# Kernel optimization log

Hardware: AMD Instinct MI355X
Metric: run time of the kernel (lower is better)

The kernel has to match this reference:

```python
import jax, jax.numpy as jnp
import numpy as np
from jax import lax

GROUPS = 8            # _resolve_groups(256, 8) == 8
EPS = 1e-5            # GroupNorm default eps
TOPK_RATIO = 0.2
MEAN_W, TOPK_W = 0.7, 0.3
DMG_THRESH = 0.5
DN = ('NCHW', 'OIHW', 'NCHW')


def _normalize(p, axis=1):
    # clamp_min(1e-8) / clamp_min(1e-8).sum().clamp_min(1e-8)
    p = jnp.maximum(p, 1e-8)
    return p / jnp.maximum(p.sum(axis=axis, keepdims=True), 1e-8)


def _conv_head(x, w1, gn_s, gn_b, w2, b2):
    # Conv3x3(no bias) -> GroupNorm(8) -> GELU(exact) -> Dropout(eval: identity) -> Conv1x1
    h = lax.conv_general_dilated(x, w1, (1, 1), 'SAME', dimension_numbers=DN)
    B, C, H, W = h.shape
    hg = h.reshape(B, GROUPS, C // GROUPS, H, W)
    mu = jnp.mean(hg, axis=(2, 3, 4), keepdims=True)
    var = jnp.var(hg, axis=(2, 3, 4), keepdims=True)
    h = ((hg - mu) * lax.rsqrt(var + EPS)).reshape(B, C, H, W)
    h = h * gn_s[None, :, None, None] + gn_b[None, :, None, None]
    h = jax.nn.gelu(h, approximate=False)
    return lax.conv_general_dilated(h, w2, (1, 1), 'SAME', dimension_numbers=DN) + b2[None, :, None, None]


def _forward(feature_map, target_mask, dw1, dgs, dgb, dw2, db2, sw1, sgs, sgb, sw2, sb2):
    dmg_logit = _conv_head(feature_map, dw1, dgs, dgb, dw2, db2)      # [B,1,H,W]
    corn_logits = _conv_head(feature_map, sw1, sgs, sgb, sw2, sb2)    # [B,2,H,W]

    # CORN dense decode: threshold probs = cumprod(sigmoid), classes = K+1
    t = jnp.cumprod(jax.nn.sigmoid(corn_logits), axis=1)              # [B,2,H,W]
    sev = jnp.concatenate([1.0 - t[:, :1], t[:, :-1] - t[:, 1:], t[:, -1:]], axis=1)  # [B,3,H,W]
    sev = _normalize(sev, axis=1)

    p_dmg = jax.nn.sigmoid(dmg_logit)                                 # [B,1,H,W]
    pix = jnp.concatenate([1.0 - p_dmg, p_dmg * sev], axis=1)         # [B,4,H,W]
    pix = _normalize(pix, axis=1)

    sev_pred = jnp.argmax(sev, axis=1) + 1                            # [B,H,W]
    pred_labels = jnp.where(p_dmg[:, 0] >= DMG_THRESH, sev_pred, 0)

    # target_mask already at feature resolution -> nearest resize is identity
    valid = target_mask > 0.5                                         # [B,1,H,W] bool
    B, C, H, W = pix.shape
    N = H * W
    flat = pix.transpose(0, 2, 3, 1).reshape(B, N, C)                 # [B,N,C]
    mf = valid.reshape(B, N)                                          # [B,N]
    cnt = mf.sum(axis=1)                                              # [B] int
    uniform = jnp.full((B, C), 1.0 / C, dtype=flat.dtype)

    # masked mean
    denom = jnp.maximum(cnt, 1).astype(flat.dtype)[:, None]
    mean_p = (flat * mf[..., None]).sum(axis=1) / denom
    mean_p = jnp.where((cnt == 0)[:, None], uniform, mean_p)
    mean_p = _normalize(mean_p, axis=1)

    # masked top-k mean via descending sort + cumsum gather (probs >= 0, invalid -> -1)
    masked = jnp.where(mf[..., None], flat, jnp.asarray(-1.0, flat.dtype))
    srt = -jnp.sort(-masked, axis=1)                                  # descending [B,N,C]
    csum = jnp.cumsum(srt, axis=1)
    k = jnp.clip(jnp.round(cnt.astype(jnp.float32) * TOPK_RATIO).astype(jnp.int32), 1, jnp.maximum(cnt, 1))
    idx = jnp.broadcast_to((k - 1)[:, None, None], (B, 1, C))
    topk_p = jnp.take_along_axis(csum, idx, axis=1)[:, 0] / k.astype(flat.dtype)[:, None]
    topk_p = jnp.where((cnt == 0)[:, None], uniform, topk_p)
    topk_p = _normalize(topk_p, axis=1)

    agg = _normalize(MEAN_W * mean_p + TOPK_W * topk_p, axis=1)
    agg_labels = jnp.argmax(agg, axis=1)

    return (dmg_logit, corn_logits, pix, pred_labels, mean_p, topk_p, agg, agg_labels)


def setup_inputs() -> dict:
    key = jax.random.key(0)
    ks = jax.random.split(key, 8)
    B, Cin, Ch, H, W = 8, 256, 256, 128, 128
    inp = {
        'feature_map': jax.random.normal(ks[0], (B, Cin, H, W), jnp.float32),
        'target_mask': jax.random.uniform(ks[1], (B, 1, H, W), jnp.float32),
        # damage head: Conv3x3 -> GN -> Conv1x1 (1 out)
        'dw1': jax.random.normal(ks[2], (Ch, Cin, 3, 3), jnp.float32) * 0.05,
        'dgs': jnp.ones((Ch,), jnp.float32),
        'dgb': jnp.zeros((Ch,), jnp.float32),
        'dw2': jax.random.normal(ks[3], (1, Ch, 1, 1), jnp.float32) * 0.05,
        'db2': jnp.zeros((1,), jnp.float32),
        # severity head: Conv3x3 -> GN -> Conv1x1 (2 thresholds)
        'sw1': jax.random.normal(ks[4], (Ch, Cin, 3, 3), jnp.float32) * 0.05,
        'sgs': jnp.ones((Ch,), jnp.float32),
        'sgb': jnp.zeros((Ch,), jnp.float32),
        'sw2': jax.random.normal(ks[5], (2, Ch, 1, 1), jnp.float32) * 0.05,
        'sb2': jnp.zeros((2,), jnp.float32),
    }
    return inp


def reference(feature_map, target_mask, dw1, dgs, dgb, dw2, db2, sw1, sgs, sgb, sw2, sb2):
    return _forward(feature_map, target_mask, dw1, dgs, dgb, dw2, db2, sw1, sgs, sgb, sw2, sb2)
```

## Files before the change

### kernel.cpp

```cpp
#include <hip/hip_runtime.h>
#include <hip/hip_bf16.h>

#define BB   8
#define CIN  256
#define CHN  256
#define HH   128
#define WWD  128
#define HW   (HH * WWD)
#define GRP_ELEMS ((size_t)32 * HW)

#define FLAG_DL   4e-3f
#define FLAG_GAP  1.5e-3f

#define BO_DSUM1   0
#define BO_DSUM2   1024
#define BO_FSTAT1  2048
#define BO_FSTAT2  2560
#define BO_DSTAT1  3072
#define BO_DSTAT2  4096
#define BO_MEAN    5120
#define BO_CNT     5248
#define BO_TOPK    5280
#define BO_FLAGC   5408
#define MEMSET_BYTES 8192
#define BO_WL      8192
#define WLCAP      32768

#define XP_OFF    139264ull
#define XP_BYTES  67108864ull
#define HB_OFF    (XP_OFF + XP_BYTES)
#define HB_BYTES  134217728ull
#define WH_OFF    (HB_OFF + HB_BYTES)
#define WT_BYTES  1179648ull
#define WL_OFF    (WH_OFF + WT_BYTES)
#define WT32_OFF  (WL_OFF + WT_BYTES)
#define WT32_BYTES 4718592ull
#define MFMA_NEED (WT32_OFF + WT32_BYTES)

#define O_DMG   0
#define O_CORN  131072
#define O_PIX   393216
#define O_LAB   917504
#define O_MEAN  1048576
#define O_TOPK  1048608
#define O_AGG   1048640
#define O_ALAB  1048672

typedef __attribute__((ext_vector_type(8))) _Float16 f16x8;
typedef __attribute__((ext_vector_type(4))) float f32x4;

__device__ inline ushort f2h(float f) {
    _Float16 h = (_Float16)f;
    union { _Float16 h; ushort u; } c; c.h = h; return c.u;
}
__device__ inline float h2f(ushort u) {
    union { ushort u; _Float16 h; } c; c.u = u; return (float)c.h;
}

__device__ inline void store4v(float* p, float a, float b, float c, float d) {
    *(float4*)p = make_float4(a, b, c, d);
}
__device__ inline void store4v(__hip_bfloat16* p, float a, float b, float c, float d) {
    p[0] = __float2bfloat16(a); p[1] = __float2bfloat16(b);
    p[2] = __float2bfloat16(c); p[3] = __float2bfloat16(d);
}
__device__ inline float ldv(const float* p) { return *p; }
__device__ inline float ldv(const __hip_bfloat16* p) { return __bfloat162float(*p); }


__global__ __launch_bounds__(256) void pack_x_f16(
    const float* __restrict__ x, ushort* __restrict__ Xh)
{
    int bid = blockIdx.x;
    int cc = bid & 7;
    int y  = (bid >> 3) & 127;
    int b  = bid >> 10;
    __shared__ ushort tile[32][137];
    const int tid = threadIdx.x;
    for (int i = tid; i < 1024; i += 256) {
        int ci = i >> 5;
        int x4 = (i & 31) << 2;
        float4 v = *(const float4*)&x[(((size_t)b * 256 + cc * 32 + ci) * 128 + y) * 128 + x4];
        tile[ci][x4 + 0] = f2h(v.x);
        tile[ci][x4 + 1] = f2h(v.y);
        tile[ci][x4 + 2] = f2h(v.z);
        tile[ci][x4 + 3] = f2h(v.w);
    }
    __syncthreads();
    ushort* dst = Xh + ((((size_t)b * 128 + y) * 8 + cc) << 12);
    for (int i = tid; i < 512; i += 256) {
        int xx  = i >> 2;
        int ci0 = (i & 3) << 3;
        ushort tmp[8];
#pragma unroll
        for (int j = 0; j < 8; j++) tmp[j] = tile[ci0 + j][xx];
        *(uint4*)&dst[i << 3] = *(uint4*)tmp;
    }
}

__global__ __launch_bounds__(256) void transpose_w(
    const float* __restrict__ w, ushort* __restrict__ Whh,
    ushort* __restrict__ Whl, float* __restrict__ Wt32)
{
    __shared__ float lt[8][33];
    int idx = blockIdx.x * 256 + threadIdx.x;
    int tap = idx >> 16;
    int rem = idx & 65535;
    int cc  = rem >> 13;
    int co  = (rem >> 5) & 255;
    int ci5 = rem & 31;
    int ci  = cc * 32 + ci5;
    float v = w[((size_t)co * 256 + ci) * 9 + tap];
    ushort h = f2h(v);
    int sidx = (((tap * 8 + cc) * 16 + (co >> 4)) << 9)
             + (((co & 15) + ((ci5 >> 3) << 4)) << 3) + (ci5 & 7);
    Whh[sidx] = h;
    Whl[sidx] = f2h(v - h2f(h));
    lt[threadIdx.x >> 5][ci5] = v;
    __syncthreads();
    int co_base = (blockIdx.x * 8) & 255;
    int ci5w = threadIdx.x >> 3;
    int j    = threadIdx.x & 7;
    Wt32[((size_t)tap * 256 + cc * 32 + ci5w) * 256 + co_base + j] = lt[j][ci5w];
}

__device__ __forceinline__ void gld16(const void* g, void* l)
{
    __builtin_amdgcn_global_load_lds(
        (const __attribute__((address_space(1))) void*)g,
        (__attribute__((address_space(3))) void*)l, 16, 0, 0);
}

__device__ __forceinline__ void issue_b_slice(
    const ushort* __restrict__ Whh, const ushort* __restrict__ Whl,
    ushort* dst, int u, int co0, int tid, int wb)
{
    const int su  = u / 3;
    const int kxu = u - su * 3;
    const int tap = ((su >> 3) * 3) + kxu;
    const int cc  = su & 7;
    const size_t sbase = ((size_t)((tap * 8 + cc) * 16 + (co0 >> 4)) << 9);
    const ushort* s0 = Whh + sbase;
    const ushort* s1 = Whl + sbase;
#pragma unroll
    for (int k = 0; k < 2; k++)
        gld16(s0 + (k * 256 + tid) * 8, dst + (size_t)(k * 256 + wb) * 8);
#pragma unroll
    for (int k = 0; k < 2; k++)
        gld16(s1 + (k * 256 + tid) * 8, dst + 4096 + (size_t)(k * 256 + wb) * 8);
}

__device__ __forceinline__ void issue_a_slice(
    const ushort* __restrict__ Xh, const ushort* __restrict__ zb,
    ushort* dst, int b, int y, int sn, int tid, int wb)
{
    const int kyn = sn >> 3, ccn = sn & 7;
    const int rown = y + kyn - 1;
    const bool rv = (unsigned)rown < 128u;
    const ushort* base = rv ? (Xh + ((((size_t)b * 128 + rown) * 8 + ccn) << 12)) : zb;
#pragma unroll
    for (int k = 0; k < 2; k++) {
        int idx = k * 256 + tid;
        int xi  = (idx + 4) >> 2;
        int q   = (idx & 3) ^ ((xi >> 1) & 3);
        int off = rv ? ((xi - 1) * 32 + q * 8) : (idx * 8);
        gld16(base + off, dst + 32 + (size_t)(k * 256 + wb) * 8);
    }
}

__global__ __launch_bounds__(256, 3) void conv3x3_mfma(
    const ushort* __restrict__ Xh, const ushort* __restrict__ Whh,
    const ushort* __restrict__ Whl, const ushort* __restrict__ zb,
    float* __restrict__ hout, double* __restrict__ sums)
{
    __shared__ ushort a_lds[2][4160];
    __shared__ ushort b_lds[2][8192];
    __shared__ float sred[8];

    const int bxr = blockIdx.x;
    const int y   = bxr >> 3;
    const int b   = bxr & 7;
    const int co0 = blockIdx.y << 7;
    const int tid  = threadIdx.x;
    const int lane = tid & 63;
    const int wb   = tid & 192;
    const int wv   = tid >> 6;
    const int m = lane & 15;
    const int q = lane >> 4;
    const int wpx = (wv & 1) << 6;
    const int wco = (wv >> 1) << 6;
    const int g0  = wco >> 4;

    if (tid < 8) sred[tid] = 0.f;
    if (tid < 16) {
        int tg = tid >> 2, p4 = tid & 3;
        ushort* r = &a_lds[tg >> 1][(tg & 1) ? (129 * 32) : 0];
        *(uint4*)(r + p4 * 8) = make_uint4(0u, 0u, 0u, 0u);
    }

    f32x4 acc[4][4];
#pragma unroll
    for (int f = 0; f < 4; f++)
#pragma unroll
        for (int g = 0; g < 4; g++) acc[f][g] = (f32x4){0.f, 0.f, 0.f, 0.f};

    issue_a_slice(Xh, zb, a_lds[0], b, y, 0, tid, wb);
    issue_b_slice(Whh, Whl, b_lds[0], 0, co0, tid, wb);
    asm volatile("s_waitcnt lgkmcnt(0)" ::: "memory");

    for (int s = 0; s < 24; s++) {
        const ushort* acur = a_lds[s & 1];
#pragma unroll
        for (int kx = 0; kx < 3; kx++) {
            const int t = 3 * s + kx;
            asm volatile("" ::: "memory");
            __builtin_amdgcn_s_barrier();
            {
                int u = t + 1;
                int ub = u & 1;
                if (u > 71) u = 71;
                issue_b_slice(Whh, Whl, b_lds[ub], u, co0, tid, wb);
            }
            if (kx == 0) {
                int sn = s + 1;
                int ab = sn & 1;
                if (sn > 23) sn = 23;
                issue_a_slice(Xh, zb, a_lds[ab], b, y, sn, tid, wb);
            }
            if (kx == 2) asm volatile("s_waitcnt vmcnt(4)" ::: "memory");
            else         asm volatile("s_waitcnt vmcnt(6)" ::: "memory");
            __builtin_amdgcn_s_barrier();
            asm volatile("" ::: "memory");

            const ushort* bb = b_lds[t & 1];
            f16x8 ah[4], bh[4], bl[4];
#pragma unroll
            for (int f = 0; f < 4; f++) {
                int row = wpx + f * 16 + kx + m;
                ah[f] = *(const f16x8*)(acur + row * 32
                        + ((q ^ ((row >> 1) & 3)) << 3));
            }
#pragma unroll
            for (int g = 0; g < 4; g++) {
                int off = ((g0 + g) << 9) + (lane << 3);
                bh[g] = *(const f16x8*)&bb[off];
                bl[g] = *(const f16x8*)&bb[4096 + off];
            }
            __builtin_amdgcn_s_setprio(1);
#pragma unroll
            for (int f = 0; f < 4; f++)
#pragma unroll
                for (int g = 0; g < 4; g++)
                    acc[f][g] = __builtin_amdgcn_mfma_f32_16x16x32_f16(ah[f], bh[g], acc[f][g], 0, 0, 0);
#pragma unroll
            for (int f = 0; f < 4; f++)
#pragma unroll
                for (int g = 0; g < 4; g++)
                    acc[f][g] = __builtin_amdgcn_mfma_f32_16x16x32_f16(ah[f], bl[g], acc[f][g], 0, 0, 0);
            __builtin_amdgcn_s_setprio(0);
        }
    }

    float s0 = 0.f, q0 = 0.f, s1 = 0.f, q1 = 0.f;
#pragma unroll
    for (int f = 0; f < 4; f++) {
#pragma unroll
        for (int g = 0; g < 4; g++) {
            f32x4 v = acc[f][g];
            float a = v.x + v.y + v.z + v.w;
            float qq = v.x * v.x + v.y * v.y + v.z * v.z + v.w * v.w;
            if (g < 2) { s0 += a; q0 += qq; } else { s1 += a; q1 += qq; }
            int px = wpx + f * 16 + q * 4;
            int co = co0 + wco + g * 16 + m;
            *(f32x4*)&hout[((size_t)(b * 256 + co) * 128 + y) * 128 + px] = v;
        }
    }
    int gl = wco >> 5;
    atomicAdd(&sred[gl],     s0);
    atomicAdd(&sred[gl + 1], s1);
    atomicAdd(&sred[4 + gl],     q0);
    atomicAdd(&sred[4 + gl + 1], q1);
    __syncthreads();
    if (tid < 4) atomicAdd(&sums[b * 8 + (co0 >> 5) + tid], (double)sred[tid]);
    else if (tid < 8) atomicAdd(&sums[64 + b * 8 + (co0 >> 5) + tid - 4], (double)sred[tid]);
}

template <typename HT>
__global__ __launch_bounds__(256) void conv3x3_gn_stats(
    const float* __restrict__ x, const float* __restrict__ w,
    HT* __restrict__ hout, double* __restrict__ sums)
{
    __shared__ float in_lds[8][3][132];
    __shared__ float w_lds[8][9][68];
    __shared__ float sred[2], qred[2];

    const int bx  = blockIdx.x;
    const int y   = bx & (HH - 1);
    const int b   = bx >> 7;
    const int co0 = blockIdx.y << 6;
    const int tid = threadIdx.x;
    if (tid < 2) { sred[tid] = 0.f; qred[tid] = 0.f; }
    const int tco = (tid & 15) << 2;
    const int tox = (tid >> 4) << 3;

    float acc[4][8];
#pragma unroll
    for (int i = 0; i < 4; i++)
#pragma unroll
        for (int j = 0; j < 8; j++) acc[i][j] = 0.f;

    const float* xb = x + (size_t)b * CIN * HW;
    for (int c0 = 0; c0 < CIN; c0 += 8) {
        __syncthreads();
        for (int i = tid; i < 8 * 3 * 130; i += 256) {
            int ci  = i / 390;
            int rem = i - ci * 390;
            int r   = rem / 130;
            int cx  = rem - r * 130;
            int gy  = y + r - 1;
            int gx  = cx - 1;
            float v = 0.f;
            if ((unsigned)gy < HH && (unsigned)gx < WWD)
                v = xb[(size_t)(c0 + ci) * HW + gy * WWD + gx];
            in_lds[ci][r][cx] = v;
        }
        for (int i = tid; i < 64 * 72; i += 256) {
            int co = i / 72;
            int kk = i - co * 72;
            int ci = kk / 9;
            int k9 = kk - ci * 9;
            w_lds[ci][k9][co] = w[((size_t)(co0 + co) * CIN + (c0 + ci)) * 9 + k9];
        }
        __syncthreads();
#pragma unroll
        for (int ci = 0; ci < 8; ci++) {
#pragma unroll
            for (int ky = 0; ky < 3; ky++) {
                const float* rowp = &in_lds[ci][ky][tox];
                float4 a0 = *(const float4*)rowp;
                float4 a1 = *(const float4*)(rowp + 4);
                float2 a2 = *(const float2*)(rowp + 8);
                float in10[10] = {a0.x, a0.y, a0.z, a0.w,
                                  a1.x, a1.y, a1.z, a1.w, a2.x, a2.y};
#pragma unroll
                for (int kx = 0; kx < 3; kx++) {
                    float4 wv = *(const float4*)&w_lds[ci][ky * 3 + kx][tco];
#pragma unroll
                    for (int ox = 0; ox < 8; ox++) {
                        float iv = in10[ox + kx];
                        acc[0][ox] = fmaf(iv, wv.x, acc[0][ox]);
                        acc[1][ox] = fmaf(iv, wv.y, acc[1][ox]);
                        acc[2][ox] = fmaf(iv, wv.z, acc[2][ox]);
                        acc[3][ox] = fmaf(iv, wv.w, acc[3][ox]);
                    }
                }
            }
        }
    }

    float s = 0.f, qv = 0.f;
#pragma unroll
    for (int oc = 0; oc < 4; oc++)
#pragma unroll
        for (int ox = 0; ox < 8; ox++) { float v = acc[oc][ox]; s += v; qv = fmaf(v, v, qv); }
#pragma unroll
    for (int oc = 0; oc < 4; oc++) {
        size_t base = ((size_t)(b * CHN + co0 + tco + oc)) * HW + y * WWD + tox;
        store4v(hout + base,     acc[oc][0], acc[oc][1], acc[oc][2], acc[oc][3]);
        store4v(hout + base + 4, acc[oc][4], acc[oc][5], acc[oc][6], acc[oc][7]);
    }
    const int gsel = tco >> 5;
    atomicAdd(&sred[gsel], s);
    atomicAdd(&qred[gsel], qv);
    __syncthreads();
    if (tid < 2) {
        int grp = (co0 >> 5) + tid;
        atomicAdd(&sums[b * 8 + grp],      (double)sred[tid]);
        atomicAdd(&sums[64 + b * 8 + grp], (double)qred[tid]);
    }
}

__global__ void gn_finalize(const double* __restrict__ dsums,
                            float* __restrict__ fstats, double* __restrict__ dstats)
{
    int i = threadIdx.x;
    if (i < 64) {
        double inv = 1.0 / (double)GRP_ELEMS;
        double mu  = dsums[i] * inv;
        double ex2 = dsums[64 + i] * inv;
        double var = ex2 - mu * mu;
        double rs  = 1.0 / sqrt(var + 1e-5);
        fstats[i]      = (float)mu;
        fstats[64 + i] = (float)rs;
        dstats[i]      = mu;
        dstats[64 + i] = rs;
    }
}

template <typename HT>
__global__ __launch_bounds__(256) void gn_head(
    const HT* __restrict__ hbuf,
    const float* __restrict__ gs, const float* __restrict__ gb,
    const float* __restrict__ w2, const float* __restrict__ b2,
    const float* __restrict__ stats,
    float* __restrict__ out, int nout)
{
    __shared__ float sc[256], sh[256], w2s[2][256];
    const int b = blockIdx.y;
    const int p = blockIdx.x * 256 + threadIdx.x;
    {
        int c = threadIdx.x;
        float mu = stats[b * 8 + (c >> 5)];
        float rs = stats[64 + b * 8 + (c >> 5)];
        float s  = gs[c] * rs;
        sc[c] = s;
        sh[c] = gb[c] - mu * s;
        w2s[0][c] = w2[c];
        w2s[1][c] = (nout > 1) ? w2[256 + c] : 0.f;
    }
    __syncthreads();
    const HT* hp = hbuf + (size_t)b * CHN * HW + p;
    float a0 = 0.f, a1 = 0.f;
#pragma unroll 4
    for (int c = 0; c < 256; c++) {
        float v = ldv(hp + (size_t)c * HW);
        v = fmaf(v, sc[c], sh[c]);
        float g = 0.5f * v * (1.f + erff(v * 0.70710678118654752440f));
        a0 = fmaf(g, w2s[0][c], a0);
        a1 = fmaf(g, w2s[1][c], a1);
    }
    out[(size_t)b * nout * HW + p] = a0 + b2[0];
    if (nout > 1) out[(size_t)b * nout * HW + HW + p] = a1 + b2[1];
}

__global__ __launch_bounds__(256) void decode_kernel(
    float* __restrict__ outw, const float* __restrict__ mask,
    float* __restrict__ meanacc, float* __restrict__ cntacc,
    int* __restrict__ flagcnt, int* __restrict__ wl)
{
    const int b = blockIdx.y;
    const int p = blockIdx.x * 256 + threadIdx.x;

    float dl = outw[O_DMG + b * HW + p];
    float c0 = outw[O_CORN + (b * 2 + 0) * HW + p];
    float c1 = outw[O_CORN + (b * 2 + 1) * HW + p];

    float s0 = 1.f / (1.f + expf(-c0));
    float s1 = 1.f / (1.f + expf(-c1));
    float t0 = s0, t1 = s0 * s1;
    float e0 = fmaxf(1.f - t0, 1e-8f);
    float e1 = fmaxf(t0 - t1, 1e-8f);
    float e2 = fmaxf(t1, 1e-8f);
    float es = fmaxf(e0 + e1 + e2, 1e-8f);
    e0 /= es; e1 /= es; e2 /= es;

    float pd = 1.f / (1.f + expf(-dl));
    float q0 = fmaxf(1.f - pd, 1e-8f);
    float q1 = fmaxf(pd * e0, 1e-8f);
    float q2 = fmaxf(pd * e1, 1e-8f);
    float q3 = fmaxf(pd * e2, 1e-8f);
    float qs = fmaxf(q0 + q1 + q2 + q3, 1e-8f);
    q0 /= qs; q1 /= qs; q2 /= qs; q3 /= qs;

    outw[O_PIX + ((size_t)b * 4 + 0) * HW + p] = q0;
    outw[O_PIX + ((size_t)b * 4 + 1) * HW + p] = q1;
    outw[O_PIX + ((size_t)b * 4 + 2) * HW + p] = q2;
    outw[O_PIX + ((size_t)b * 4 + 3) * HW + p] = q3;

    int am = 0; float bv = e0;
    if (e1 > bv) { bv = e1; am = 1; }
    if (e2 > bv) { bv = e2; am = 2; }
    outw[O_LAB + b * HW + p] = (pd >= 0.5f) ? (float)(am + 1) : 0.f;

    bool flag = (fabsf(dl) < FLAG_DL);
    {
        float top1 = e0, top2 = fmaxf(e1, e2);
        if (e1 > top1) { top1 = e1; top2 = fmaxf(e0, e2); }
        if (e2 > top1) { top1 = e2; top2 = fmaxf(e0, e1); }
        if ((top1 - top2 < FLAG_GAP) && (dl > -FLAG_DL)) flag = true;
    }
    if (flag) {
        int idx = atomicAdd(flagcnt, 1);
        if (idx < WLCAP) wl[idx] = b * HW + p;
    }

    bool valid = mask[b * HW + p] > 0.5f;
    float vm = valid ? 1.f : 0.f;
    float v0 = valid ? q0 : 0.f, v1 = valid ? q1 : 0.f;
    float v2 = valid ? q2 : 0.f, v3 = valid ? q3 : 0.f;

#pragma unroll
    for (int o = 32; o; o >>= 1) {
        v0 += __shfl_down(v0, o); v1 += __shfl_down(v1, o);
        v2 += __shfl_down(v2, o); v3 += __shfl_down(v3, o);
        vm += __shfl_down(vm, o);
    }
    __shared__ float racc[5];
    if (threadIdx.x < 5) racc[threadIdx.x] = 0.f;
    __syncthreads();
    if ((threadIdx.x & 63) == 0) {
        atomicAdd(&racc[0], v0); atomicAdd(&racc[1], v1);
        atomicAdd(&racc[2], v2); atomicAdd(&racc[3], v3);
        atomicAdd(&racc[4], vm);
    }
    __syncthreads();
    if (threadIdx.x < 4) atomicAdd(&meanacc[b * 4 + threadIdx.x], racc[threadIdx.x]);
    if (threadIdx.x == 4) atomicAdd(&cntacc[b], racc[4]);
}

__global__ __launch_bounds__(256) void fixup_labels(
    const float* __restrict__ x, const float* __restrict__ Wt32,
    const float* __restrict__ dgs, const float* __restrict__ dgb,
    const float* __restrict__ dw2, const float* __restrict__ db2,
    const float* __restrict__ sgs, const float* __restrict__ sgb,
    const float* __restrict__ sw2, const float* __restrict__ sb2,
    const double* __restrict__ dstat1, const double* __restrict__ dstat2,
    const int* __restrict__ wl, const int* __restrict__ wcnt,
    float* __restrict__ out)
{
    __shared__ float xp[2304];
    __shared__ double dpart[4][256];
    __shared__ double wred[3][4];

    int count = *wcnt;
    if (count > WLCAP) count = WLCAP;
    const int tid  = threadIdx.x;
    const int lane = tid & 63;
    const int wv   = tid >> 6;
    const int c4   = lane << 2;
    const int j0   = wv * 576;

    for (int pix = blockIdx.x; pix < count; pix += gridDim.x) {
        __syncthreads();
        const int pid = wl[pix];
        const int b = pid >> 14, yy = (pid >> 7) & 127, xx = pid & 127;
        for (int i = tid; i < 2304; i += 256) {
            int t = i >> 8, ci = i & 255;
            int ky = t / 3, kx = t - ky * 3;
            int gy = yy + ky - 1, gx = xx + kx - 1;
            float v = 0.f;
            if ((unsigned)gy < 128u && (unsigned)gx < 128u)
                v = x[(((size_t)b * 256 + ci) * 128 + gy) * 128 + gx];
            xp[i] = v;
        }
        __syncthreads();

        for (int head = 0; head < 2; head++) {
            const float* gs  = head ? sgs : dgs;
            const float* gb  = head ? sgb : dgb;
            const float* w2  = head ? sw2 : dw2;
            const double* st = head ? dstat2 : dstat1;
            const float* wt  = Wt32 + (size_t)head * 589824;

            double a0 = 0.0, a1 = 0.0, a2 = 0.0, a3 = 0.0;
            for (int jc = 0; jc < 576; jc += 8) {
                float4 wv4[8];
#pragma unroll
                for (int u = 0; u < 8; u++)
                    wv4[u] = *(const float4*)&wt[(size_t)(j0 + jc + u) * 256 + c4];
#pragma unroll
                for (int u = 0; u < 8; u++) {
                    double xv = (double)xp[j0 + jc + u];
                    a0 += xv * (double)wv4[u].x;
                    a1 += xv * (double)wv4[u].y;
                    a2 += xv * (double)wv4[u].z;
                    a3 += xv * (double)wv4[u].w;
                }
            }
            dpart[wv][c4]     = a0;
            dpart[wv][c4 + 1] = a1;
            dpart[wv][c4 + 2] = a2;
            dpart[wv][c4 + 3] = a3;
            __syncthreads();

            {
                const int c = tid;
                double h = dpart[0][c] + dpart[1][c] + dpart[2][c] + dpart[3][c];
                double mu = st[b * 8 + (c >> 5)];
                double rs = st[64 + b * 8 + (c >> 5)];
                double v = (h - mu) * rs * (double)gs[c] + (double)gb[c];
                double g = 0.5 * v * (1.0 + erf(v * 0.70710678118654752440));
                double r0 = g * (double)w2[c];
#pragma unroll
                for (int o = 32; o; o >>= 1) r0 += __shfl_down(r0, o);
                if (lane == 0) wred[head][wv] = r0;
                if (head == 1) {
                    double r1 = g * (double)w2[256 + c];
#pragma unroll
                    for (int o = 32; o; o >>= 1) r1 += __shfl_down(r1, o);
                    if (lane == 0) wred[2][wv] = r1;
                }
            }
            __syncthreads();
        }

        if (tid == 0) {
            double dlv = wred[0][0] + wred[0][1] + wred[0][2] + wred[0][3] + (double)db2[0];
            double c0v = wred[1][0] + wred[1][1] + wred[1][2] + wred[1][3] + (double)sb2[0];
            double c1v = wred[2][0] + wred[2][1] + wred[2][2] + wred[2][3] + (double)sb2[1];
            double s0 = 1.0 / (1.0 + exp(-c0v));
            double s1 = 1.0 / (1.0 + exp(-c1v));
            double t0 = s0, t1 = s0 * s1;
            double e0 = fmax(1.0 - t0, 1e-8);
            double e1 = fmax(t0 - t1, 1e-8);
            double e2 = fmax(t1, 1e-8);
            int am = 0; double bv = e0;
            if (e1 > bv) { bv = e1; am = 1; }
            if (e2 > bv) { bv = e2; am = 2; }
            out[O_LAB + pid] = (dlv >= 0.0) ? (float)(am + 1) : 0.f;
        }
    }
}

__global__ __launch_bounds__(256) void topk_kernel(
    const float* __restrict__ outw, const float* __restrict__ mask,
    const float* __restrict__ cntacc, float* __restrict__ topkout)
{
    const int b = blockIdx.x >> 2;
    const int c = blockIdx.x & 3;
    const int tid = threadIdx.x;

    __shared__ int hist[256];
    __shared__ unsigned s_prefix;
    __shared__ int s_want;
    __shared__ float s_red[4];
    __shared__ int s_redi[4];

    float cntf = cntacc[b];
    int cnt = (int)cntf;
    int k = (int)rintf(cntf * 0.2f);
    if (k < 1) k = 1;
    int kmax = cnt > 1 ? cnt : 1;
    if (k > kmax) k = kmax;

    if (tid == 0) { s_prefix = 0u; s_want = k; }

    const float* pv = outw + O_PIX + ((size_t)b * 4 + c) * HW;
    const float* pm = mask + (size_t)b * HW;

    unsigned uv[64];
#pragma unroll
    for (int j = 0; j < 64; j++) {
        int p = tid + (j << 8);
        float v = (pm[p] > 0.5f) ? pv[p] : -1.0f;
        unsigned bits = __float_as_uint(v);
        uv[j] = (bits & 0x80000000u) ? ~bits : (bits | 0x80000000u);
    }

    for (int pass = 0; pass < 4; pass++) {
        hist[tid] = 0;
        __syncthreads();
        const int shift = 24 - 8 * pass;
        const unsigned pmask = pass ? (0xFFFFFFFFu << (shift + 8)) : 0u;
        const unsigned prefix = s_prefix;
#pragma unroll
        for (int j = 0; j < 64; j++) {
            unsigned u = uv[j];
            if ((u & pmask) == prefix) atomicAdd(&hist[(u >> shift) & 255], 1);
        }
        __syncthreads();
        if (tid == 0) {
            int want = s_want;
            int bin = 255;
            while (bin > 0) {
                int h = hist[bin];
                if (want <= h) break;
                want -= h;
                bin--;
            }
            s_want = want;
            s_prefix = prefix | ((unsigned)bin << shift);
        }
        __syncthreads();
    }
    const unsigned tau = s_prefix;

    float sgt = 0.f; int cgt = 0;
#pragma unroll
    for (int j = 0; j < 64; j++) {
        unsigned u = uv[j];
        if (u > tau) {
            unsigned bits = (u & 0x80000000u) ? (u & 0x7FFFFFFFu) : ~u;
            sgt += __uint_as_float(bits);
            cgt++;
        }
    }
#pragma unroll
    for (int o = 32; o; o >>= 1) { sgt += __shfl_down(sgt, o); cgt += __shfl_down(cgt, o); }
    if ((tid & 63) == 0) { s_red[tid >> 6] = sgt; s_redi[tid >> 6] = cgt; }
    __syncthreads();
    if (tid == 0) {
        float S = s_red[0] + s_red[1] + s_red[2] + s_red[3];
        int   C = s_redi[0] + s_redi[1] + s_redi[2] + s_redi[3];
        unsigned tb = (tau & 0x80000000u) ? (tau & 0x7FFFFFFFu) : ~tau;
        float tf = __uint_as_float(tb);
        float total = S + (float)(k - C) * tf;
        topkout[b * 4 + c] = total / (float)k;
    }
}

__device__ inline void norm4(float* p)
{
    float a = fmaxf(p[0], 1e-8f), b = fmaxf(p[1], 1e-8f);
    float c = fmaxf(p[2], 1e-8f), d = fmaxf(p[3], 1e-8f);
    float s = fmaxf(a + b + c + d, 1e-8f);
    p[0] = a / s; p[1] = b / s; p[2] = c / s; p[3] = d / s;
}

__global__ void final_kernel(const float* __restrict__ meanacc,
                             const float* __restrict__ cntacc,
                             const float* __restrict__ topkv,
                             float* __restrict__ outw)
{
    int b = threadIdx.x;
    if (b >= 8) return;
    float cnt = cntacc[b];
    bool zero = (cnt == 0.f);
    float denom = fmaxf(cnt, 1.f);
    float m[4], t[4], a[4];
#pragma unroll
    for (int c = 0; c < 4; c++) {
        m[c] = zero ? 0.25f : meanacc[b * 4 + c] / denom;
        t[c] = zero ? 0.25f : topkv[b * 4 + c];
    }
    norm4(m); norm4(t);
#pragma unroll
    for (int c = 0; c < 4; c++) a[c] = 0.7f * m[c] + 0.3f * t[c];
    norm4(a);
    int am = 0; float bv = a[0];
#pragma unroll
    for (int c = 1; c < 4; c++) if (a[c] > bv) { bv = a[c]; am = c; }
#pragma unroll
    for (int c = 0; c < 4; c++) {
        outw[O_MEAN + b * 4 + c] = m[c];
        outw[O_TOPK + b * 4 + c] = t[c];
        outw[O_AGG  + b * 4 + c] = a[c];
    }
    outw[O_ALAB + b] = (float)am;
}

extern "C" void kernel_launch(void* const* d_in, const int* in_sizes, int n_in,
                              void* d_out, int out_size, void* d_ws, size_t ws_size,
                              hipStream_t stream)
{
    (void)in_sizes; (void)n_in; (void)out_size;
    const float* x    = (const float*)d_in[0];
    const float* mask = (const float*)d_in[1];
    const float* dw1  = (const float*)d_in[2];
    const float* dgs  = (const float*)d_in[3];
    const float* dgb  = (const float*)d_in[4];
    const float* dw2  = (const float*)d_in[5];
    const float* db2  = (const float*)d_in[6];
    const float* sw1  = (const float*)d_in[7];
    const float* sgs  = (const float*)d_in[8];
    const float* sgb  = (const float*)d_in[9];
    const float* sw2  = (const float*)d_in[10];
    const float* sb2  = (const float*)d_in[11];
    float* out = (float*)d_out;

    char* wsb = (char*)d_ws;
    double* dsum1  = (double*)(wsb + BO_DSUM1);
    double* dsum2  = (double*)(wsb + BO_DSUM2);
    float*  fstat1 = (float*)(wsb + BO_FSTAT1);
    float*  fstat2 = (float*)(wsb + BO_FSTAT2);
    double* dstat1 = (double*)(wsb + BO_DSTAT1);
    double* dstat2 = (double*)(wsb + BO_DSTAT2);
    float*  meanacc = (float*)(wsb + BO_MEAN);
    float*  cntacc  = (float*)(wsb + BO_CNT);
    float*  topkv   = (float*)(wsb + BO_TOPK);
    int*    flagc   = (int*)(wsb + BO_FLAGC);
    int*    wl      = (int*)(wsb + BO_WL);

    hipMemsetAsync(d_ws, 0, MEMSET_BYTES + 8192, stream);

    dim3 pgrid(64, BB);

    if (ws_size >= MFMA_NEED) {
        ushort* Xh   = (ushort*)(wsb + XP_OFF);
        float*  hb   = (float*)(wsb + HB_OFF);
        ushort* Whh  = (ushort*)(wsb + WH_OFF);
        ushort* Whl  = (ushort*)(wsb + WL_OFF);
        float*  Wt32 = (float*)(wsb + WT32_OFF);
        const ushort* zb = (const ushort*)(wsb + BO_WL);

        pack_x_f16<<<8192, 256, 0, stream>>>(x, Xh);

        dim3 cgrid(1024, 2);
        transpose_w<<<2304, 256, 0, stream>>>(dw1, Whh, Whl, Wt32);
        conv3x3_mfma<<<cgrid, 256, 0, stream>>>(Xh, Whh, Whl, zb, hb, dsum1);
        gn_finalize<<<1, 64, 0, stream>>>(dsum1, fstat1, dstat1);
        gn_head<float><<<pgrid, 256, 0, stream>>>(hb, dgs, dgb, dw2, db2,
                                                  fstat1, out + O_DMG, 1);
        transpose_w<<<2304, 256, 0, stream>>>(sw1, Whh, Whl, Wt32 + 589824);
        conv3x3_mfma<<<cgrid, 256, 0, stream>>>(Xh, Whh, Whl, zb, hb, dsum2);
        gn_finalize<<<1, 64, 0, stream>>>(dsum2, fstat2, dstat2);
        gn_head<float><<<pgrid, 256, 0, stream>>>(hb, sgs, sgb, sw2, sb2,
                                                  fstat2, out + O_CORN, 2);

        decode_kernel<<<pgrid, 256, 0, stream>>>(out, mask, meanacc, cntacc, flagc, wl);
        fixup_labels<<<512, 256, 0, stream>>>(x, Wt32, dgs, dgb, dw2, db2,
                                              sgs, sgb, sw2, sb2,
                                              dstat1, dstat2, wl, flagc, out);
        topk_kernel<<<32, 256, 0, stream>>>(out, mask, cntacc, topkv);
        final_kernel<<<1, 64, 0, stream>>>(meanacc, cntacc, topkv, out);
    } else {
        void* hbuf = wsb + XP_OFF;
        dim3 cgrid(HH * BB, CHN / 64);
        const size_t needF32 = XP_OFF + (size_t)BB * CHN * HW * sizeof(float);
        if (ws_size >= needF32) {
            conv3x3_gn_stats<float><<<cgrid, 256, 0, stream>>>(x, dw1, (float*)hbuf, dsum1);
            gn_finalize<<<1, 64, 0, stream>>>(dsum1, fstat1, dstat1);
            gn_head<float><<<pgrid, 256, 0, stream>>>((float*)hbuf, dgs, dgb, dw2, db2,
                                                      fstat1, out + O_DMG, 1);
            conv3x3_gn_stats<float><<<cgrid, 256, 0, stream>>>(x, sw1, (float*)hbuf, dsum2);
            gn_finalize<<<1, 64, 0, stream>>>(dsum2, fstat2, dstat2);
            gn_head<float><<<pgrid, 256, 0, stream>>>((float*)hbuf, sgs, sgb, sw2, sb2,
                                                      fstat2, out + O_CORN, 2);
        } else {
            conv3x3_gn_stats<__hip_bfloat16><<<cgrid, 256, 0, stream>>>(x, dw1, (__hip_bfloat16*)hbuf, dsum1);
            gn_finalize<<<1, 64, 0, stream>>>(dsum1, fstat1, dstat1);
            gn_head<__hip_bfloat16><<<pgrid, 256, 0, stream>>>((__hip_bfloat16*)hbuf, dgs, dgb, dw2, db2,
                                                               fstat1, out + O_DMG, 1);
            conv3x3_gn_stats<__hip_bfloat16><<<cgrid, 256, 0, stream>>>(x, sw1, (__hip_bfloat16*)hbuf, dsum2);
            gn_finalize<<<1, 64, 0, stream>>>(dsum2, fstat2, dstat2);
            gn_head<__hip_bfloat16><<<pgrid, 256, 0, stream>>>((__hip_bfloat16*)hbuf, sgs, sgb, sw2, sb2,
                                                               fstat2, out + O_CORN, 2);
        }
        decode_kernel<<<pgrid, 256, 0, stream>>>(out, mask, meanacc, cntacc, flagc, wl);
        topk_kernel<<<32, 256, 0, stream>>>(out, mask, cntacc, topkv);
        final_kernel<<<1, 64, 0, stream>>>(meanacc, cntacc, topkv, out);
    }
}
```

Before: 1.260 ms.

## Merge both conv heads into one MFMA launch with separate hidden buffers

Both 3x3 conv heads now run in a single MFMA kernel launch with four column tiles: two per head, each with its own weights and hidden buffer. GroupNorm finalize and the GN/GELU/1x1 head also each run once for both heads. This removes serialized launches and the tail idle time between the two convs, and it doubles the grid so the GPU is kept busier. The cost is a second 128 MB hidden buffer, which raises workspace demand and memory traffic. The per-channel loop unroll also goes from 4 to 16.

```diff
diff --git a/kernel.cpp b/kernel.cpp
--- a/kernel.cpp
+++ b/kernel.cpp
@@ -31,11 +31,14 @@
 #define HB_OFF    (XP_OFF + XP_BYTES)
 #define HB_BYTES  134217728ull
 #define WH_OFF    (HB_OFF + HB_BYTES)
-#define WT_BYTES  1179648ull
-#define WL_OFF    (WH_OFF + WT_BYTES)
-#define WT32_OFF  (WL_OFF + WT_BYTES)
+#define WT1_ELEMS 589824
+#define WH2_BYTES 2359296ull
+#define WL2_OFF   (WH_OFF + WH2_BYTES)
+#define WT32_OFF  (WL2_OFF + WH2_BYTES)
 #define WT32_BYTES 4718592ull
-#define MFMA_NEED (WT32_OFF + WT32_BYTES)
+#define HB2_OFF   (WT32_OFF + WT32_BYTES)
+#define NEED_B    (WT32_OFF + WT32_BYTES)
+#define NEED_A    (HB2_OFF + HB_BYTES)
 
 #define O_DMG   0
 #define O_CORN  131072
@@ -168,10 +171,12 @@
     }
 }
 
+template <int MERGED>
 __global__ __launch_bounds__(256, 3) void conv3x3_mfma(
     const ushort* __restrict__ Xh, const ushort* __restrict__ Whh,
     const ushort* __restrict__ Whl, const ushort* __restrict__ zb,
-    float* __restrict__ hout, double* __restrict__ sums)
+    float* __restrict__ hb1, float* __restrict__ hb2,
+    double* __restrict__ sums, int headfix)
 {
     __shared__ ushort a_lds[2][4160];
     __shared__ ushort b_lds[2][8192];
@@ -180,7 +185,14 @@
     const int bxr = blockIdx.x;
     const int y   = bxr >> 3;
     const int b   = bxr & 7;
-    const int co0 = blockIdx.y << 7;
+    const int by  = blockIdx.y;
+    const int head = MERGED ? (by >> 1) : headfix;
+    const int co0  = MERGED ? ((by & 1) << 7) : (by << 7);
+    const ushort* WhhH = Whh + head * WT1_ELEMS;
+    const ushort* WhlH = Whl + head * WT1_ELEMS;
+    float* hout = head ? hb2 : hb1;
+    double* sumsH = sums + head * 128;
+
     const int tid  = threadIdx.x;
     const int lane = tid & 63;
     const int wb   = tid & 192;
@@ -205,7 +217,7 @@
         for (int g = 0; g < 4; g++) acc[f][g] = (f32x4){0.f, 0.f, 0.f, 0.f};
 
     issue_a_slice(Xh, zb, a_lds[0], b, y, 0, tid, wb);
-    issue_b_slice(Whh, Whl, b_lds[0], 0, co0, tid, wb);
+    issue_b_slice(WhhH, WhlH, b_lds[0], 0, co0, tid, wb);
     asm volatile("s_waitcnt lgkmcnt(0)" ::: "memory");
 
     for (int s = 0; s < 24; s++) {
@@ -219,7 +231,7 @@
                 int u = t + 1;
                 int ub = u & 1;
                 if (u > 71) u = 71;
-                issue_b_slice(Whh, Whl, b_lds[ub], u, co0, tid, wb);
+                issue_b_slice(WhhH, WhlH, b_lds[ub], u, co0, tid, wb);
             }
             if (kx == 0) {
                 int sn = s + 1;
@@ -281,8 +293,8 @@
     atomicAdd(&sred[4 + gl],     q0);
     atomicAdd(&sred[4 + gl + 1], q1);
     __syncthreads();
-    if (tid < 4) atomicAdd(&sums[b * 8 + (co0 >> 5) + tid], (double)sred[tid]);
-    else if (tid < 8) atomicAdd(&sums[64 + b * 8 + (co0 >> 5) + tid - 4], (double)sred[tid]);
+    if (tid < 4) atomicAdd(&sumsH[b * 8 + (co0 >> 5) + tid], (double)sred[tid]);
+    else if (tid < 8) atomicAdd(&sumsH[64 + b * 8 + (co0 >> 5) + tid - 4], (double)sred[tid]);
 }
 
 template <typename HT>
@@ -397,6 +409,24 @@
     }
 }
 
+__global__ void gn_finalize_all(const double* __restrict__ dsums,
+                                float* __restrict__ fstats, double* __restrict__ dstats)
+{
+    int i = threadIdx.x;
+    if (i < 128) {
+        int head = i >> 6, j = i & 63;
+        double inv = 1.0 / (double)GRP_ELEMS;
+        double mu  = dsums[head * 128 + j] * inv;
+        double ex2 = dsums[head * 128 + 64 + j] * inv;
+        double var = ex2 - mu * mu;
+        double rs  = 1.0 / sqrt(var + 1e-5);
+        fstats[head * 128 + j]      = (float)mu;
+        fstats[head * 128 + 64 + j] = (float)rs;
+        dstats[head * 128 + j]      = mu;
+        dstats[head * 128 + 64 + j] = rs;
+    }
+}
+
 template <typename HT>
 __global__ __launch_bounds__(256) void gn_head(
     const HT* __restrict__ hbuf,
@@ -421,7 +451,7 @@
     __syncthreads();
     const HT* hp = hbuf + (size_t)b * CHN * HW + p;
     float a0 = 0.f, a1 = 0.f;
-#pragma unroll 4
+#pragma unroll 16
     for (int c = 0; c < 256; c++) {
         float v = ldv(hp + (size_t)c * HW);
         v = fmaf(v, sc[c], sh[c]);
@@ -431,6 +461,53 @@
     }
     out[(size_t)b * nout * HW + p] = a0 + b2[0];
     if (nout > 1) out[(size_t)b * nout * HW + HW + p] = a1 + b2[1];
+}
+
+__global__ __launch_bounds__(256) void gn_head_m(
+    const float* __restrict__ hb1, const float* __restrict__ hb2,
+    const float* __restrict__ dgs, const float* __restrict__ dgb,
+    const float* __restrict__ dw2, const float* __restrict__ db2,
+    const float* __restrict__ sgs, const float* __restrict__ sgb,
+    const float* __restrict__ sw2, const float* __restrict__ sb2,
+    const float* __restrict__ fstats, float* __restrict__ out)
+{
+    __shared__ float sc[256], sh[256], w2s[2][256];
+    const int head = blockIdx.z;
+    const float* hbuf = head ? hb2 : hb1;
+    const float* gs = head ? sgs : dgs;
+    const float* gb = head ? sgb : dgb;
+    const float* w2 = head ? sw2 : dw2;
+    const float* b2 = head ? sb2 : db2;
+    const float* stats = fstats + head * 128;
+    const int b = blockIdx.y;
+    const int p = blockIdx.x * 256 + threadIdx.x;
+    {
+        int c = threadIdx.x;
+        float mu = stats[b * 8 + (c >> 5)];
+        float rs = stats[64 + b * 8 + (c >> 5)];
+        float s  = gs[c] * rs;
+        sc[c] = s;
+        sh[c] = gb[c] - mu * s;
+        w2s[0][c] = w2[c];
+        w2s[1][c] = head ? w2[256 + c] : 0.f;
+    }
+    __syncthreads();
+    const float* hp = hbuf + (size_t)b * CHN * HW + p;
+    float a0 = 0.f, a1 = 0.f;
+#pragma unroll 16
+    for (int c = 0; c < 256; c++) {
+        float v = hp[(size_t)c * HW];
+        v = fmaf(v, sc[c], sh[c]);
+        float g = 0.5f * v * (1.f + erff(v * 0.70710678118654752440f));
+        a0 = fmaf(g, w2s[0][c], a0);
+        a1 = fmaf(g, w2s[1][c], a1);
+    }
+    if (head == 0) {
+        out[O_DMG + (size_t)b * HW + p] = a0 + b2[0];
+    } else {
+        out[O_CORN + (size_t)b * 2 * HW + p]      = a0 + b2[0];
+        out[O_CORN + (size_t)b * 2 * HW + HW + p] = a1 + b2[1];
+    }
 }
 
 __global__ __launch_bounds__(256) void decode_kernel(
@@ -775,27 +852,38 @@
 
     dim3 pgrid(64, BB);
 
-    if (ws_size >= MFMA_NEED) {
+    if (ws_size >= NEED_B) {
         ushort* Xh   = (ushort*)(wsb + XP_OFF);
-        float*  hb   = (float*)(wsb + HB_OFF);
+        float*  hb1  = (float*)(wsb + HB_OFF);
         ushort* Whh  = (ushort*)(wsb + WH_OFF);
-        ushort* Whl  = (ushort*)(wsb + WL_OFF);
+        ushort* Whl  = (ushort*)(wsb + WL2_OFF);
         float*  Wt32 = (float*)(wsb + WT32_OFF);
         const ushort* zb = (const ushort*)(wsb + BO_WL);
 
         pack_x_f16<<<8192, 256, 0, stream>>>(x, Xh);
-
-        dim3 cgrid(1024, 2);
         transpose_w<<<2304, 256, 0, stream>>>(dw1, Whh, Whl, Wt32);
-        conv3x3_mfma<<<cgrid, 256, 0, stream>>>(Xh, Whh, Whl, zb, hb, dsum1);
-        gn_finalize<<<1, 64, 0, stream>>>(dsum1, fstat1, dstat1);
-        gn_head<float><<<pgrid, 256, 0, stream>>>(hb, dgs, dgb, dw2, db2,
-                                                  fstat1, out + O_DMG, 1);
-        transpose_w<<<2304, 256, 0, stream>>>(sw1, Whh, Whl, Wt32 + 589824);
-        conv3x3_mfma<<<cgrid, 256, 0, stream>>>(Xh, Whh, Whl, zb, hb, dsum2);
-        gn_finalize<<<1, 64, 0, stream>>>(dsum2, fstat2, dstat2);
-        gn_head<float><<<pgrid, 256, 0, stream>>>(hb, sgs, sgb, sw2, sb2,
-                                                  fstat2, out + O_CORN, 2);
+        transpose_w<<<2304, 256, 0, stream>>>(sw1, Whh + WT1_ELEMS, Whl + WT1_ELEMS,
+                                              Wt32 + WT1_ELEMS);
+
+        if (ws_size >= NEED_A) {
+            float* hb2 = (float*)(wsb + HB2_OFF);
+            conv3x3_mfma<1><<<dim3(1024, 4), 256, 0, stream>>>(
+                Xh, Whh, Whl, zb, hb1, hb2, dsum1, 0);
+            gn_finalize_all<<<1, 128, 0, stream>>>(dsum1, fstat1, dstat1);
+            gn_head_m<<<dim3(64, BB, 2), 256, 0, stream>>>(
+                hb1, hb2, dgs, dgb, dw2, db2, sgs, sgb, sw2, sb2, fstat1, out);
+        } else {
+            conv3x3_mfma<0><<<dim3(1024, 2), 256, 0, stream>>>(
+                Xh, Whh, Whl, zb, hb1, hb1, dsum1, 0);
+            gn_finalize<<<1, 64, 0, stream>>>(dsum1, fstat1, dstat1);
+            gn_head<float><<<pgrid, 256, 0, stream>>>(hb1, dgs, dgb, dw2, db2,
+                                                      fstat1, out + O_DMG, 1);
+            conv3x3_mfma<0><<<dim3(1024, 2), 256, 0, stream>>>(
+                Xh, Whh, Whl, zb, hb1, hb1, dsum1, 1);
+            gn_finalize<<<1, 64, 0, stream>>>(dsum2, fstat2, dstat2);
+            gn_head<float><<<pgrid, 256, 0, stream>>>(hb1, sgs, sgb, sw2, sb2,
+                                                      fstat2, out + O_CORN, 2);
+        }
 
         decode_kernel<<<pgrid, 256, 0, stream>>>(out, mask, meanacc, cntacc, flagc, wl);
         fixup_labels<<<512, 256, 0, stream>>>(x, Wt32, dgs, dgb, dw2, db2,
```

After: 1.255 ms. No clear change (-0.4%).
